# Kernel tuning notes

Hardware: AMD Instinct MI355X
Metric: run time of the kernel (lower is better)

## Reference

```python
import jax, jax.numpy as jnp
import numpy as np

BS, NCAM, CIN, H, W = 1, 6, 512, 32, 88
MID = 256
DBINS = 112  # (58 - 2) / 0.5
VX, VY, VZ = 128, 128, 16


def conv2d(x, w, pad=1):
    return jax.lax.conv_general_dilated(
        x, w, (1, 1), [(pad, pad), (pad, pad)],
        dimension_numbers=('NCHW', 'OIHW', 'NCHW'))


def grid_sample_3d(feat, grid):
    """F.grid_sample 3D, bilinear, padding_mode='zeros', align_corners=False.
    feat: (N, C, D, H, W); grid: (N, X, Y, Z, 3) with xyz -> (W, H, D) coords in [-1,1].
    Returns (N, C, X, Y, Z)."""
    N, C, D, Hh, Ww = feat.shape
    gx, gy, gz = grid[..., 0], grid[..., 1], grid[..., 2]
    ix = ((gx + 1.0) * Ww - 1.0) * 0.5
    iy = ((gy + 1.0) * Hh - 1.0) * 0.5
    iz = ((gz + 1.0) * D - 1.0) * 0.5
    ix0, iy0, iz0 = jnp.floor(ix), jnp.floor(iy), jnp.floor(iz)
    fx, fy, fz = ix - ix0, iy - iy0, iz - iz0
    feat_flat = feat.reshape(N, C, D * Hh * Ww)
    out = jnp.zeros((N, C) + grid.shape[1:-1], feat.dtype)
    for dz in (0, 1):
        for dy in (0, 1):
            for dx in (0, 1):
                xi, yi, zi = ix0 + dx, iy0 + dy, iz0 + dz
                w_ = ((fx if dx else 1.0 - fx) * (fy if dy else 1.0 - fy)
                      * (fz if dz else 1.0 - fz))
                valid = ((xi >= 0) & (xi < Ww) & (yi >= 0) & (yi < Hh)
                         & (zi >= 0) & (zi < D))
                xc = jnp.clip(xi, 0, Ww - 1).astype(jnp.int32)
                yc = jnp.clip(yi, 0, Hh - 1).astype(jnp.int32)
                zc = jnp.clip(zi, 0, D - 1).astype(jnp.int32)
                idx = ((zc * Hh + yc) * Ww + xc).reshape(N, 1, -1)
                g = jnp.take_along_axis(feat_flat, idx, axis=2)
                g = g.reshape((N, C) + grid.shape[1:-1])
                out = out + g * (w_ * valid)[:, None]
    return out


def setup_inputs():
    key = jax.random.key(0)
    ks = jax.random.split(key, 16)
    f32 = jnp.float32
    img_feat = jax.random.normal(ks[0], (BS, NCAM, CIN, H, W), f32)
    intr = np.zeros((NCAM, 4, 4), np.float32)
    for i in range(NCAM):
        f = 1266.0 + 10.0 * i
        intr[i, 0, 0] = f; intr[i, 1, 1] = f
        intr[i, 0, 2] = 800.0; intr[i, 1, 2] = 450.0
        intr[i, 2, 2] = 1.0; intr[i, 3, 3] = 1.0
    intrins = jnp.asarray(intr)[None]  # (1, 6, 4, 4)
    # normalized frustum-sample coords; slightly beyond [-1,1] to hit zero padding
    grid = jax.random.uniform(ks[1], (BS, NCAM, VX, VY, VZ, 3), f32, -1.1, 1.1)
    s3 = (2.0 / (CIN * 9)) ** 0.5
    sm = (2.0 / (MID * 9)) ** 0.5
    s1 = (2.0 / MID) ** 0.5
    red_w = jax.random.normal(ks[2], (MID, CIN, 3, 3), f32) * s3
    red_s = jnp.ones((MID,), f32); red_b = jnp.zeros((MID,), f32)
    mlp_w1 = jax.random.normal(ks[3], (1, MID), f32) * 1.4
    mlp_b1 = jnp.zeros((MID,), f32)
    mlp_w2 = jax.random.normal(ks[4], (MID, MID), f32) * s1
    mlp_b2 = jnp.zeros((MID,), f32)
    se_rw = jax.random.normal(ks[5], (MID, MID, 1, 1), f32) * s1
    se_rb = jnp.zeros((MID,), f32)
    se_ew = jax.random.normal(ks[6], (MID, MID, 1, 1), f32) * s1
    se_eb = jnp.zeros((MID,), f32)
    bb_w = jax.random.normal(ks[7], (3, 2, MID, MID, 3, 3), f32) * sm
    bb_s = jnp.ones((3, 2, MID), f32); bb_b = jnp.zeros((3, 2, MID), f32)
    dp_w = jax.random.normal(ks[8], (DBINS, MID, 1, 1), f32) * s1
    dp_b = jnp.zeros((DBINS,), f32)
    return dict(img_feat=img_feat, intrins=intrins, grid=grid,
                red_w=red_w, red_s=red_s, red_b=red_b,
                mlp_w1=mlp_w1, mlp_b1=mlp_b1, mlp_w2=mlp_w2, mlp_b2=mlp_b2,
                se_rw=se_rw, se_rb=se_rb, se_ew=se_ew, se_eb=se_eb,
                bb_w=bb_w, bb_s=bb_s, bb_b=bb_b, dp_w=dp_w, dp_b=dp_b)


def reference(img_feat, intrins, grid, red_w, red_s, red_b,
              mlp_w1, mlp_b1, mlp_w2, mlp_b2,
              se_rw, se_rb, se_ew, se_eb, bb_w, bb_s, bb_b, dp_w, dp_b):
    bs, n, c, h, w = img_feat.shape
    x = img_feat.reshape(bs * n, c, h, w)
    # pixel-size SE conditioning from inverse intrinsics
    inv = jnp.linalg.inv(intrins)
    pixel_size = jnp.linalg.norm(
        jnp.stack([inv[..., 0, 0], inv[..., 1, 1]], -1), axis=-1).reshape(-1, 1)
    sp = pixel_size * 1000.0  # scale_depth_factor
    # reduce_conv: conv3x3 + (folded) BN + ReLU
    x = conv2d(x, red_w)
    x = jax.nn.relu(x * red_s[:, None, None] + red_b[:, None, None])
    # Mlp on scaled pixel size
    x_se = jax.nn.relu(sp @ mlp_w1 + mlp_b1) @ mlp_w2 + mlp_b2
    x_se = x_se[:, :, None, None]
    # SELayer
    t = jax.nn.relu(conv2d(x_se, se_rw, pad=0) + se_rb[:, None, None])
    gate = jax.nn.sigmoid(conv2d(t, se_ew, pad=0) + se_eb[:, None, None])
    x = x * gate
    # 3 BasicBlocks (conv-bn-relu-conv-bn + residual, relu), BN folded (eval)
    for i in range(3):
        y = conv2d(x, bb_w[i, 0])
        y = jax.nn.relu(y * bb_s[i, 0][:, None, None] + bb_b[i, 0][:, None, None])
        y = conv2d(y, bb_w[i, 1])
        y = y * bb_s[i, 1][:, None, None] + bb_b[i, 1][:, None, None]
        x = jax.nn.relu(x + y)
    depth = conv2d(x, dp_w, pad=0) + dp_b[:, None, None]  # (bs*n, D, h, w)
    dp = jax.nn.softmax(depth, axis=1)
    # stack depth prob and ones so one grid_sample yields features AND voxel mask
    feat = jnp.stack([dp, jnp.ones_like(dp)], axis=1)  # (bs*n, 2, D, h, w)
    g = grid.reshape((bs * n,) + grid.shape[2:])       # (bs*n, X, Y, Z, 3)
    sampled = grid_sample_3d(feat, g)                  # (bs*n, 2, X, Y, Z)
    sampled = sampled.reshape((bs, n) + sampled.shape[1:]).sum(axis=1)
    agg, masks = sampled[:, :1], sampled[:, 1:]
    out = jnp.where(masks > 0, agg / jnp.where(masks > 0, masks, 1.0), agg)
    return out  # (bs, 1, X, Y, Z)
```

## Files before the change

kernel.cpp:

```cpp
#include <hip/hip_runtime.h>

typedef _Float16 f16;
typedef _Float16 f16x8 __attribute__((ext_vector_type(8)));
typedef _Float16 f16x4 __attribute__((ext_vector_type(4)));
typedef float f32x4 __attribute__((ext_vector_type(4)));

#define NCAM 6
#define CINF 512
#define MIDC 256
#define DB   112
#define HH   32
#define WW   88
#define PH   34
#define PW   90
#define NPOS (HH*WW)
#define PTILE 64
#define PT_PER_CAM 44

#define O_GATE   0L
#define O_WFRED  6144L
#define O_LOG    6144L
#define O_WFBB   2365440L
#define O_WFDP   9443328L
#define O_XP0    9508864L
#define O_X1     28309504L
#define O_DP     28309504L
#define O_X2     37709824L
#define O_X3     47110144L

__device__ __forceinline__ void gl_lds16(const void* g, void* l) {
  __builtin_amdgcn_global_load_lds((const __attribute__((address_space(1))) void*)g,
                                   (__attribute__((address_space(3))) void*)l, 16, 0, 0);
}

__global__ void halo_zero_kernel(f16* __restrict__ xp0, f16* __restrict__ X1,
                                 f16* __restrict__ X2, f16* __restrict__ X3) {
  int idx = blockIdx.x * 256 + threadIdx.x;
  f16* base; int C, rem;
  if (idx < 93696) { base = xp0; C = 512; rem = idx; }
  else {
    int k = idx - 93696;
    int bsel = k / 46848;
    if (bsel >= 3) return;
    rem = k - bsel * 46848; C = 256;
    base = (bsel == 0) ? X1 : (bsel == 1) ? X2 : X3;
  }
  int chunks = C >> 3;
  int cell = rem / chunks, cc = rem - cell * chunks;
  int cam = cell / 244, p = cell - cam * 244;
  int hh, ww;
  if (p < 90)       { hh = 0;  ww = p; }
  else if (p < 180) { hh = 33; ww = p - 90; }
  else { int q = p - 180; hh = 1 + (q >> 1); ww = (q & 1) * 89; }
  long o = ((long)(cam * PH + hh) * PW + ww) * C + cc * 8;
  f16x8 z = {0,0,0,0,0,0,0,0};
  *(f16x8*)(base + o) = z;
}

__global__ void wfrag_kernel(const float* __restrict__ src, const float* __restrict__ scale,
                             f16* __restrict__ dst, int NC, int G, int TAPS, int CI, int CO_SRC,
                             long per, long total) {
  long i = (long)blockIdx.x * blockDim.x + threadIdx.x;
  long stride = (long)gridDim.x * blockDim.x;
  int KST = CI >> 5;
  for (; i < total; i += stride) {
    int conv = (int)(i / per);
    long rem = i - (long)conv * per;
    int j = (int)(rem & 7);
    int lane = (int)((rem >> 3) & 63);
    int mi = (int)((rem >> 9) & 3);
    long b = rem >> 11;
    int ks = (int)(b % KST);
    long b2 = b / KST;
    int tap = (int)(b2 % TAPS);
    int g = (int)(b2 / TAPS);
    int co = g * 64 + mi * 16 + (lane & 15);
    int ci = ks * 32 + (lane >> 4) * 8 + j;
    float v = 0.f;
    if (co < CO_SRC) {
      v = src[(long)conv * CO_SRC * CI * TAPS + ((long)co * CI + ci) * TAPS + tap];
      if (scale) v *= scale[conv * CO_SRC + co];
    }
    dst[i] = (f16)v;
  }
}

__global__ void img_trans_kernel(const float* __restrict__ src, f16* __restrict__ dst) {
  __shared__ float tile[32][33];
  int tx = threadIdx.x & 31, ty = threadIdx.x >> 5;
  int wt = blockIdx.x % 3, ct = blockIdx.x / 3;
  int h = blockIdx.y, n = blockIdx.z;
  int w0 = wt * 32, c0 = ct * 32;
  #pragma unroll
  for (int i = 0; i < 4; ++i) {
    int cl = ty + i * 8;
    int w = w0 + tx;
    float v = 0.f;
    if (w < WW) v = src[((long)(n * CINF + c0 + cl) * HH + h) * WW + w];
    tile[cl][tx] = v;
  }
  __syncthreads();
  #pragma unroll
  for (int i = 0; i < 4; ++i) {
    int wl = ty + i * 8;
    int w = w0 + wl;
    if (w < WW)
      dst[((long)((n * PH + h + 1) * PW + (w + 1))) * CINF + c0 + tx] = (f16)tile[tx][wl];
  }
}

__global__ void se_gate_kernel(const float* __restrict__ intr,
                               const float* __restrict__ w1, const float* __restrict__ b1,
                               const float* __restrict__ w2, const float* __restrict__ b2,
                               const float* __restrict__ rw, const float* __restrict__ rb,
                               const float* __restrict__ ew, const float* __restrict__ eb,
                               float* __restrict__ gate) {
  __shared__ float sps;
  __shared__ float h1[MIDC];
  __shared__ float h2[MIDC];
  __shared__ float tt[MIDC];
  int n = blockIdx.x, c = threadIdx.x;
  if (c == 0) {
    float a[4][8];
    for (int i = 0; i < 4; ++i)
      for (int j = 0; j < 4; ++j) {
        a[i][j] = intr[n * 16 + i * 4 + j];
        a[i][4 + j] = (i == j) ? 1.f : 0.f;
      }
    for (int col = 0; col < 4; ++col) {
      int piv = col;
      for (int r2 = col + 1; r2 < 4; ++r2)
        if (fabsf(a[r2][col]) > fabsf(a[piv][col])) piv = r2;
      if (piv != col)
        for (int j = 0; j < 8; ++j) { float tv = a[col][j]; a[col][j] = a[piv][j]; a[piv][j] = tv; }
      float invp = 1.f / a[col][col];
      for (int j = 0; j < 8; ++j) a[col][j] *= invp;
      for (int r2 = 0; r2 < 4; ++r2)
        if (r2 != col) {
          float f = a[r2][col];
          for (int j = 0; j < 8; ++j) a[r2][j] -= f * a[col][j];
        }
    }
    float i00 = a[0][4], i11 = a[1][5];
    sps = sqrtf(i00 * i00 + i11 * i11) * 1000.f;
  }
  __syncthreads();
  float sp = sps;
  h1[c] = fmaxf(sp * w1[c] + b1[c], 0.f);
  __syncthreads();
  float acc = b2[c];
  for (int j = 0; j < MIDC; ++j) acc += h1[j] * w2[j * MIDC + c];
  h2[c] = acc;
  __syncthreads();
  acc = rb[c];
  for (int j = 0; j < MIDC; ++j) acc += rw[c * MIDC + j] * h2[j];
  tt[c] = fmaxf(acc, 0.f);
  __syncthreads();
  acc = eb[c];
  for (int j = 0; j < MIDC; ++j) acc += ew[c * MIDC + j] * tt[j];
  gate[n * MIDC + c] = 1.f / (1.f + expf(-acc));
}

template<int MODE, int CIN_T, int TAPS>
__global__ __launch_bounds__(256, 2)
void conv_mfma(const f16* __restrict__ X, const f16* __restrict__ Wf,
               const float* __restrict__ bias, const float* __restrict__ gate,
               const f16* __restrict__ res, f16* __restrict__ Yf16,
               float* __restrict__ Yf32, int co_tiles) {
  constexpr int KST = CIN_T / 32;
  constexpr int CPT = CIN_T / 64;
  constexpr int NCH = TAPS * CPT;
  constexpr int LCPT = (CPT == 8) ? 3 : 2;
  constexpr long GSTR = (long)TAPS * KST * 4096;
  __shared__ __align__(16) char S[49152];

  const int t = threadIdx.x;
  const int wv = t >> 6, ln = t & 63, lm = ln & 15, quad = ln >> 4;
  const int wm = wv >> 1, wn = wv & 1;
  const int bid0 = blockIdx.x;
  const int cpx = gridDim.x >> 3;
  const int bid = (bid0 & 7) * cpx + (bid0 >> 3);
  const int co_tile = bid % co_tiles;
  const int ptile = bid / co_tiles;
  const int cam = ptile / PT_PER_CAM;
  const int pbase = (ptile % PT_PER_CAM) * PTILE;

  const f16* gB[2]; int ldsoffB[2];
  const int clog = (ln & 7) ^ (ln >> 3);
  #pragma unroll
  for (int j = 0; j < 2; ++j) {
    int reg = j * 4 + wv;
    int r = reg * 8 + (ln >> 3);
    int pos = pbase + r;
    int hh = pos / WW, w2 = pos - hh * WW;
    gB[j] = X + ((long)((cam * PH + hh + 1) * PW + (w2 + 1))) * CIN_T + clog * 8;
    ldsoffB[j] = 16384 + reg * 1024;
  }

  const int base_l = (wn * 32 + lm) * 128;
  const int sx0 = ((0 * 4 + quad) ^ (lm & 7)) * 16;
  const int sx1 = ((1 * 4 + quad) ^ (lm & 7)) * 16;

  f32x4 acc[4][2];
  #pragma unroll
  for (int mi = 0; mi < 4; ++mi)
    #pragma unroll
    for (int ni = 0; ni < 2; ++ni)
      #pragma unroll
      for (int r = 0; r < 4; ++r) acc[mi][ni][r] = 0.f;

  auto choff = [&](int c) -> long {
    long off = 0;
    if (TAPS == 9) {
      int tp = c >> LCPT;
      int dy = tp / 3 - 1, dx = tp % 3 - 1;
      off = (long)(dy * PW + dx) * CIN_T;
    }
    return off + (long)(c & (CPT - 1)) * 64;
  };
  auto stageA = [&](int bsel, int c) {
    const char* sb = (const char*)Wf + (long)c * 8192 + (long)ln * 16;
    char* db = S + bsel * 24576;
    #pragma unroll
    for (int j = 0; j < 4; ++j) {
      int seg = j * 4 + wv;
      long gb = (long)(co_tile * 2 + (seg >> 3)) * GSTR;
      gl_lds16(sb + gb + (seg & 7) * 1024, db + seg * 1024);
    }
  };
  auto stageB = [&](int bsel, long curf) {
    #pragma unroll
    for (int j = 0; j < 2; ++j)
      gl_lds16(gB[j] + curf, S + bsel * 24576 + ldsoffB[j]);
  };
  auto compute = [&](int bsel) {
    const char* ab = S + bsel * 24576 + wm * 8192 + ln * 16;
    const char* bb = S + bsel * 24576 + 16384 + base_l;
    #pragma unroll
    for (int s = 0; s < 2; ++s) {
      f16x8 af[4];
      #pragma unroll
      for (int mi = 0; mi < 4; ++mi)
        af[mi] = *(const f16x8*)(ab + s * 4096 + mi * 1024);
      f16x8 bf[2];
      int sx = s ? sx1 : sx0;
      #pragma unroll
      for (int ni = 0; ni < 2; ++ni)
        bf[ni] = *(const f16x8*)(bb + ni * 2048 + sx);
      #pragma unroll
      for (int mi = 0; mi < 4; ++mi)
        #pragma unroll
        for (int ni = 0; ni < 2; ++ni)
          acc[mi][ni] = __builtin_amdgcn_mfma_f32_16x16x32_f16(af[mi], bf[ni], acc[mi][ni], 0, 0, 0);
    }
  };

  stageA(0, 0);
  stageB(0, choff(0));
  __syncthreads();

  #pragma unroll 1
  for (int c = 0; c < NCH; ++c) {
    int cur = c & 1;
    if (c + 1 < NCH) { stageA(cur ^ 1, c + 1); stageB(cur ^ 1, choff(c + 1)); }
    compute(cur);
    __syncthreads();
  }

  float4 b4[4], g4[4];
  bool skip[4];
  #pragma unroll
  for (int mi = 0; mi < 4; ++mi) {
    int co_l = wm * 64 + mi * 16 + quad * 4;
    int co_g = co_tile * 128 + co_l;
    skip[mi] = (MODE == 3) && (co_l >= DB);
    if (!skip[mi]) b4[mi] = *(const float4*)(bias + co_g);
    if (MODE == 0) g4[mi] = *(const float4*)(gate + cam * MIDC + co_g);
  }
  #pragma unroll
  for (int ni = 0; ni < 2; ++ni) {
    int pos = pbase + wn * 32 + ni * 16 + lm;
    long ob;
    if (MODE == 3) ob = ((long)(cam * NPOS + pos)) * DB;
    else {
      int hh = pos / WW, w2 = pos - hh * WW;
      ob = ((long)((cam * PH + hh + 1) * PW + (w2 + 1))) * MIDC + co_tile * 128;
    }
    #pragma unroll
    for (int mi = 0; mi < 4; ++mi) {
      if (skip[mi]) continue;
      int co_l = wm * 64 + mi * 16 + quad * 4;
      float v[4];
      #pragma unroll
      for (int r = 0; r < 4; ++r) {
        float y = acc[mi][ni][r];
        y += ((float*)&b4[mi])[r];
        if (MODE == 0) y = fmaxf(y, 0.f) * ((float*)&g4[mi])[r];
        else if (MODE == 1) y = fmaxf(y, 0.f);
        v[r] = y;
      }
      if (MODE == 3) {
        float4 o; o.x = v[0]; o.y = v[1]; o.z = v[2]; o.w = v[3];
        *(float4*)(Yf32 + ob + co_l) = o;
      } else if (MODE == 2) {
        f16x4 rv = *(const f16x4*)(res + ob + co_l);
        f16x4 o;
        #pragma unroll
        for (int r = 0; r < 4; ++r) o[r] = (f16)fmaxf(v[r] + (float)rv[r], 0.f);
        *(f16x4*)(Yf16 + ob + co_l) = o;
      } else {
        f16x4 o;
        #pragma unroll
        for (int r = 0; r < 4; ++r) o[r] = (f16)v[r];
        *(f16x4*)(Yf16 + ob + co_l) = o;
      }
    }
  }
}

__global__ void softmax_kernel(const float* __restrict__ L, float* __restrict__ dp) {
  int wid = (int)(((long)blockIdx.x * blockDim.x + threadIdx.x) >> 6);
  int lane = threadIdx.x & 63;
  if (wid >= NCAM * NPOS) return;
  const float* lp = L + (long)wid * DB;
  float v0 = -1e30f, v1 = -1e30f;
  if (lane < 56) { v0 = lp[lane * 2]; v1 = lp[lane * 2 + 1]; }
  float m = fmaxf(v0, v1);
  #pragma unroll
  for (int o = 32; o; o >>= 1) m = fmaxf(m, __shfl_xor(m, o));
  float e0 = 0.f, e1 = 0.f;
  if (lane < 56) { e0 = __expf(v0 - m); e1 = __expf(v1 - m); }
  float ssum = e0 + e1;
  #pragma unroll
  for (int o = 32; o; o >>= 1) ssum += __shfl_xor(ssum, o);
  float inv = 1.f / ssum;
  if (lane < 56) {
    float2 r; r.x = e0 * inv; r.y = e1 * inv;
    *(float2*)(dp + (long)wid * DB + lane * 2) = r;
  }
}

__global__ void sample_kernel(const float* __restrict__ grid, const float* __restrict__ dp,
                              float* __restrict__ out) {
  int v = blockIdx.x * blockDim.x + threadIdx.x;
  if (v >= 128 * 128 * 16) return;
  int vz = v & 15, vy = (v >> 4) & 127, vx = v >> 11;
  float agg = 0.f, msk = 0.f;
  #pragma unroll 1
  for (int n = 0; n < NCAM; ++n) {
    long gb = ((long)((n * 128 + vx) * 128 + vy) * 16 + vz) * 3;
    float gx = grid[gb], gy = grid[gb + 1], gz = grid[gb + 2];
    float ix = ((gx + 1.f) * (float)WW - 1.f) * 0.5f;
    float iy = ((gy + 1.f) * (float)HH - 1.f) * 0.5f;
    float iz = ((gz + 1.f) * (float)DB - 1.f) * 0.5f;
    float xf = floorf(ix), yf = floorf(iy), zf = floorf(iz);
    float fx = ix - xf, fy = iy - yf, fz = iz - zf;
    int x0 = (int)xf, y0 = (int)yf, z0 = (int)zf;
    float wxa[2] = {1.f - fx, fx};
    float wya[2] = {1.f - fy, fy};
    float wza[2] = {1.f - fz, fz};
    #pragma unroll
    for (int dy2 = 0; dy2 < 2; ++dy2) {
      int y = y0 + dy2;
      bool vyb = (y >= 0) && (y < HH);
      int yc = y < 0 ? 0 : (y > HH - 1 ? HH - 1 : y);
      #pragma unroll
      for (int dx2 = 0; dx2 < 2; ++dx2) {
        int x = x0 + dx2;
        bool vxb = (x >= 0) && (x < WW);
        int xc = x < 0 ? 0 : (x > WW - 1 ? WW - 1 : x);
        float wxy = wxa[dx2] * wya[dy2];
        const float* base = dp + ((long)((n * HH + yc) * WW + xc)) * DB;
        #pragma unroll
        for (int dz2 = 0; dz2 < 2; ++dz2) {
          int z = z0 + dz2;
          bool vzb = (z >= 0) && (z < DB);
          int zc = z < 0 ? 0 : (z > DB - 1 ? DB - 1 : z);
          float wgt = wxy * wza[dz2];
          if (vxb && vyb && vzb) {
            msk += wgt;
            agg += wgt * base[zc];
          }
        }
      }
    }
  }
  out[v] = (msk > 0.f) ? (agg / msk) : agg;
}

extern "C" void kernel_launch(void* const* d_in, const int* in_sizes, int n_in,
                              void* d_out, int out_size, void* d_ws, size_t ws_size,
                              hipStream_t stream) {
  const float* img   = (const float*)d_in[0];
  const float* intr  = (const float*)d_in[1];
  const float* grid  = (const float*)d_in[2];
  const float* red_w = (const float*)d_in[3];
  const float* red_s = (const float*)d_in[4];
  const float* red_b = (const float*)d_in[5];
  const float* w1    = (const float*)d_in[6];
  const float* b1    = (const float*)d_in[7];
  const float* w2    = (const float*)d_in[8];
  const float* b2    = (const float*)d_in[9];
  const float* rw    = (const float*)d_in[10];
  const float* rb    = (const float*)d_in[11];
  const float* ew    = (const float*)d_in[12];
  const float* eb    = (const float*)d_in[13];
  const float* bb_w  = (const float*)d_in[14];
  const float* bb_s  = (const float*)d_in[15];
  const float* bb_b  = (const float*)d_in[16];
  const float* dp_w  = (const float*)d_in[17];
  const float* dp_b  = (const float*)d_in[18];
  float* out = (float*)d_out;

  char* ws = (char*)d_ws;
  float* gate = (float*)(ws + O_GATE);
  f16* wfred  = (f16*)(ws + O_WFRED);
  f16* wfbb   = (f16*)(ws + O_WFBB);
  f16* wfdp   = (f16*)(ws + O_WFDP);
  f16* xp0    = (f16*)(ws + O_XP0);
  f16* X1     = (f16*)(ws + O_X1);
  f16* X2     = (f16*)(ws + O_X2);
  f16* X3     = (f16*)(ws + O_X3);
  float* Lg   = (float*)(ws + O_LOG);
  float* dpb  = (float*)(ws + O_DP);

  halo_zero_kernel<<<915, 256, 0, stream>>>(xp0, X1, X2, X3);
  {
    long per = 4L * 9 * 16 * 2048, total = per;
    wfrag_kernel<<<2048, 256, 0, stream>>>(red_w, red_s, wfred, 1, 4, 9, 512, 256, per, total);
  }
  {
    long per = 4L * 9 * 8 * 2048, total = 6 * per;
    wfrag_kernel<<<4096, 256, 0, stream>>>(bb_w, bb_s, wfbb, 6, 4, 9, 256, 256, per, total);
  }
  {
    long per = 2L * 1 * 8 * 2048, total = per;
    wfrag_kernel<<<128, 256, 0, stream>>>(dp_w, nullptr, wfdp, 1, 2, 1, 256, 112, per, total);
  }
  img_trans_kernel<<<dim3(48, 32, 6), 256, 0, stream>>>(img, xp0);
  se_gate_kernel<<<6, 256, 0, stream>>>(intr, w1, b1, w2, b2, rw, rb, ew, eb, gate);

  const long WCH = 4L * 9 * 8 * 2048;

  conv_mfma<0, 512, 9><<<528, 256, 0, stream>>>(xp0, wfred, red_b, gate, nullptr, X1, nullptr, 2);

  conv_mfma<1, 256, 9><<<528, 256, 0, stream>>>(X1, wfbb + 0 * WCH, bb_b + 0 * 256, nullptr, nullptr, X2, nullptr, 2);
  conv_mfma<2, 256, 9><<<528, 256, 0, stream>>>(X2, wfbb + 1 * WCH, bb_b + 1 * 256, nullptr, X1, X3, nullptr, 2);
  conv_mfma<1, 256, 9><<<528, 256, 0, stream>>>(X3, wfbb + 2 * WCH, bb_b + 2 * 256, nullptr, nullptr, X2, nullptr, 2);
  conv_mfma<2, 256, 9><<<528, 256, 0, stream>>>(X2, wfbb + 3 * WCH, bb_b + 3 * 256, nullptr, X3, X1, nullptr, 2);
  conv_mfma<1, 256, 9><<<528, 256, 0, stream>>>(X1, wfbb + 4 * WCH, bb_b + 4 * 256, nullptr, nullptr, X2, nullptr, 2);
  conv_mfma<2, 256, 9><<<528, 256, 0, stream>>>(X2, wfbb + 5 * WCH, bb_b + 5 * 256, nullptr, X1, X3, nullptr, 2);

  conv_mfma<3, 256, 1><<<264, 256, 0, stream>>>(X3, wfdp, dp_b, nullptr, nullptr, nullptr, Lg, 1);

  softmax_kernel<<<4224, 256, 0, stream>>>(Lg, dpb);
  sample_kernel<<<1024, 256, 0, stream>>>(grid, dpb, out);
}
```

Before: 483.3 us.

## Merge prep kernels into one launch and fuse softmax into depth conv epilogue

Folds halo zeroing, weight fragment packing, image transpose and SE gate into a single block-dispatched prep kernel, removing five kernel launches. The depth 1x1 conv epilogue now stages logits in LDS and computes the per-pixel softmax directly, writing probabilities and dropping the separate softmax kernel and its logit round-trip through global memory. The softmax epilogue uses only 4 lanes per pixel with strided, uncoalesced output stores.

```diff
diff --git a/kernel.cpp b/kernel.cpp
--- a/kernel.cpp
+++ b/kernel.cpp
@@ -19,7 +19,6 @@
 
 #define O_GATE   0L
 #define O_WFRED  6144L
-#define O_LOG    6144L
 #define O_WFBB   2365440L
 #define O_WFDP   9443328L
 #define O_XP0    9508864L
@@ -33,35 +32,11 @@
                                    (__attribute__((address_space(3))) void*)l, 16, 0, 0);
 }
 
-__global__ void halo_zero_kernel(f16* __restrict__ xp0, f16* __restrict__ X1,
-                                 f16* __restrict__ X2, f16* __restrict__ X3) {
-  int idx = blockIdx.x * 256 + threadIdx.x;
-  f16* base; int C, rem;
-  if (idx < 93696) { base = xp0; C = 512; rem = idx; }
-  else {
-    int k = idx - 93696;
-    int bsel = k / 46848;
-    if (bsel >= 3) return;
-    rem = k - bsel * 46848; C = 256;
-    base = (bsel == 0) ? X1 : (bsel == 1) ? X2 : X3;
-  }
-  int chunks = C >> 3;
-  int cell = rem / chunks, cc = rem - cell * chunks;
-  int cam = cell / 244, p = cell - cam * 244;
-  int hh, ww;
-  if (p < 90)       { hh = 0;  ww = p; }
-  else if (p < 180) { hh = 33; ww = p - 90; }
-  else { int q = p - 180; hh = 1 + (q >> 1); ww = (q & 1) * 89; }
-  long o = ((long)(cam * PH + hh) * PW + ww) * C + cc * 8;
-  f16x8 z = {0,0,0,0,0,0,0,0};
-  *(f16x8*)(base + o) = z;
-}
-
-__global__ void wfrag_kernel(const float* __restrict__ src, const float* __restrict__ scale,
-                             f16* __restrict__ dst, int NC, int G, int TAPS, int CI, int CO_SRC,
-                             long per, long total) {
-  long i = (long)blockIdx.x * blockDim.x + threadIdx.x;
-  long stride = (long)gridDim.x * blockDim.x;
+__device__ void wfrag_body(const float* __restrict__ src, const float* __restrict__ scale,
+                           f16* __restrict__ dst, int TAPS, int CI, int CO_SRC,
+                           long per, long total, int lbid, int nb) {
+  long i = (long)lbid * 256 + threadIdx.x;
+  long stride = (long)nb * 256;
   int KST = CI >> 5;
   for (; i < total; i += stride) {
     int conv = (int)(i / per);
@@ -85,80 +60,123 @@
   }
 }
 
-__global__ void img_trans_kernel(const float* __restrict__ src, f16* __restrict__ dst) {
-  __shared__ float tile[32][33];
-  int tx = threadIdx.x & 31, ty = threadIdx.x >> 5;
-  int wt = blockIdx.x % 3, ct = blockIdx.x / 3;
-  int h = blockIdx.y, n = blockIdx.z;
-  int w0 = wt * 32, c0 = ct * 32;
-  #pragma unroll
-  for (int i = 0; i < 4; ++i) {
-    int cl = ty + i * 8;
-    int w = w0 + tx;
-    float v = 0.f;
-    if (w < WW) v = src[((long)(n * CINF + c0 + cl) * HH + h) * WW + w];
-    tile[cl][tx] = v;
-  }
-  __syncthreads();
-  #pragma unroll
-  for (int i = 0; i < 4; ++i) {
-    int wl = ty + i * 8;
-    int w = w0 + wl;
-    if (w < WW)
-      dst[((long)((n * PH + h + 1) * PW + (w + 1))) * CINF + c0 + tx] = (f16)tile[tx][wl];
-  }
-}
-
-__global__ void se_gate_kernel(const float* __restrict__ intr,
-                               const float* __restrict__ w1, const float* __restrict__ b1,
-                               const float* __restrict__ w2, const float* __restrict__ b2,
-                               const float* __restrict__ rw, const float* __restrict__ rb,
-                               const float* __restrict__ ew, const float* __restrict__ eb,
-                               float* __restrict__ gate) {
-  __shared__ float sps;
-  __shared__ float h1[MIDC];
-  __shared__ float h2[MIDC];
-  __shared__ float tt[MIDC];
-  int n = blockIdx.x, c = threadIdx.x;
-  if (c == 0) {
-    float a[4][8];
-    for (int i = 0; i < 4; ++i)
-      for (int j = 0; j < 4; ++j) {
-        a[i][j] = intr[n * 16 + i * 4 + j];
-        a[i][4 + j] = (i == j) ? 1.f : 0.f;
+__global__ void prep_kernel(f16* __restrict__ xp0, f16* __restrict__ X1,
+                            f16* __restrict__ X2, f16* __restrict__ X3,
+                            const float* __restrict__ img,
+                            const float* __restrict__ intr,
+                            const float* __restrict__ w1, const float* __restrict__ b1,
+                            const float* __restrict__ w2, const float* __restrict__ b2,
+                            const float* __restrict__ rw, const float* __restrict__ rb,
+                            const float* __restrict__ ew, const float* __restrict__ eb,
+                            float* __restrict__ gate,
+                            const float* __restrict__ red_w, const float* __restrict__ red_s,
+                            f16* __restrict__ wfred,
+                            const float* __restrict__ bb_w, const float* __restrict__ bb_s,
+                            f16* __restrict__ wfbb,
+                            const float* __restrict__ dp_w, f16* __restrict__ wfdp) {
+  __shared__ float shbuf[1056];
+  const int bid = blockIdx.x;
+  if (bid < 915) {
+    int idx = bid * 256 + threadIdx.x;
+    f16* base; int C, rem;
+    if (idx < 93696) { base = xp0; C = 512; rem = idx; }
+    else {
+      int k = idx - 93696;
+      int bsel = k / 46848;
+      if (bsel >= 3) return;
+      rem = k - bsel * 46848; C = 256;
+      base = (bsel == 0) ? X1 : (bsel == 1) ? X2 : X3;
+    }
+    int chunks = C >> 3;
+    int cell = rem / chunks, cc = rem - cell * chunks;
+    int cam = cell / 244, p = cell - cam * 244;
+    int hh, ww;
+    if (p < 90)       { hh = 0;  ww = p; }
+    else if (p < 180) { hh = 33; ww = p - 90; }
+    else { int q = p - 180; hh = 1 + (q >> 1); ww = (q & 1) * 89; }
+    long o = ((long)(cam * PH + hh) * PW + ww) * C + cc * 8;
+    f16x8 z = {0,0,0,0,0,0,0,0};
+    *(f16x8*)(base + o) = z;
+  } else if (bid < 10131) {
+    int lb = bid - 915;
+    int x = lb % 48;
+    int h = (lb / 48) % 32;
+    int n = lb / 1536;
+    int wt = x % 3, ct = x / 3;
+    float (*tile)[33] = (float(*)[33])shbuf;
+    int tx = threadIdx.x & 31, ty = threadIdx.x >> 5;
+    int w0 = wt * 32, c0 = ct * 32;
+    #pragma unroll
+    for (int i = 0; i < 4; ++i) {
+      int cl = ty + i * 8;
+      int w = w0 + tx;
+      float v = 0.f;
+      if (w < WW) v = img[((long)(n * CINF + c0 + cl) * HH + h) * WW + w];
+      tile[cl][tx] = v;
+    }
+    __syncthreads();
+    #pragma unroll
+    for (int i = 0; i < 4; ++i) {
+      int wl = ty + i * 8;
+      int w = w0 + wl;
+      if (w < WW)
+        xp0[((long)((n * PH + h + 1) * PW + (w + 1))) * CINF + c0 + tx] = (f16)tile[tx][wl];
+    }
+  } else if (bid < 10137) {
+    int n = bid - 10131, c = threadIdx.x;
+    float* sps = shbuf;
+    float* h1 = shbuf + 32;
+    float* h2 = shbuf + 288;
+    float* tt = shbuf + 544;
+    if (c == 0) {
+      float a[4][8];
+      for (int i = 0; i < 4; ++i)
+        for (int j = 0; j < 4; ++j) {
+          a[i][j] = intr[n * 16 + i * 4 + j];
+          a[i][4 + j] = (i == j) ? 1.f : 0.f;
+        }
+      for (int col = 0; col < 4; ++col) {
+        int piv = col;
+        for (int r2 = col + 1; r2 < 4; ++r2)
+          if (fabsf(a[r2][col]) > fabsf(a[piv][col])) piv = r2;
+        if (piv != col)
+          for (int j = 0; j < 8; ++j) { float tv = a[col][j]; a[col][j] = a[piv][j]; a[piv][j] = tv; }
+        float invp = 1.f / a[col][col];
+        for (int j = 0; j < 8; ++j) a[col][j] *= invp;
+        for (int r2 = 0; r2 < 4; ++r2)
+          if (r2 != col) {
+            float f = a[r2][col];
+            for (int j = 0; j < 8; ++j) a[r2][j] -= f * a[col][j];
+          }
       }
-    for (int col = 0; col < 4; ++col) {
-      int piv = col;
-      for (int r2 = col + 1; r2 < 4; ++r2)
-        if (fabsf(a[r2][col]) > fabsf(a[piv][col])) piv = r2;
-      if (piv != col)
-        for (int j = 0; j < 8; ++j) { float tv = a[col][j]; a[col][j] = a[piv][j]; a[piv][j] = tv; }
-      float invp = 1.f / a[col][col];
-      for (int j = 0; j < 8; ++j) a[col][j] *= invp;
-      for (int r2 = 0; r2 < 4; ++r2)
-        if (r2 != col) {
-          float f = a[r2][col];
-          for (int j = 0; j < 8; ++j) a[r2][j] -= f * a[col][j];
-        }
-    }
-    float i00 = a[0][4], i11 = a[1][5];
-    sps = sqrtf(i00 * i00 + i11 * i11) * 1000.f;
-  }
-  __syncthreads();
-  float sp = sps;
-  h1[c] = fmaxf(sp * w1[c] + b1[c], 0.f);
-  __syncthreads();
-  float acc = b2[c];
-  for (int j = 0; j < MIDC; ++j) acc += h1[j] * w2[j * MIDC + c];
-  h2[c] = acc;
-  __syncthreads();
-  acc = rb[c];
-  for (int j = 0; j < MIDC; ++j) acc += rw[c * MIDC + j] * h2[j];
-  tt[c] = fmaxf(acc, 0.f);
-  __syncthreads();
-  acc = eb[c];
-  for (int j = 0; j < MIDC; ++j) acc += ew[c * MIDC + j] * tt[j];
-  gate[n * MIDC + c] = 1.f / (1.f + expf(-acc));
+      float i00 = a[0][4], i11 = a[1][5];
+      sps[0] = sqrtf(i00 * i00 + i11 * i11) * 1000.f;
+    }
+    __syncthreads();
+    float sp = sps[0];
+    h1[c] = fmaxf(sp * w1[c] + b1[c], 0.f);
+    __syncthreads();
+    float acc = b2[c];
+    for (int j = 0; j < MIDC; ++j) acc += h1[j] * w2[j * MIDC + c];
+    h2[c] = acc;
+    __syncthreads();
+    acc = rb[c];
+    for (int j = 0; j < MIDC; ++j) acc += rw[c * MIDC + j] * h2[j];
+    tt[c] = fmaxf(acc, 0.f);
+    __syncthreads();
+    acc = eb[c];
+    for (int j = 0; j < MIDC; ++j) acc += ew[c * MIDC + j] * tt[j];
+    gate[n * MIDC + c] = 1.f / (1.f + expf(-acc));
+  } else if (bid < 12185) {
+    long per = 4L * 9 * 16 * 2048;
+    wfrag_body(red_w, red_s, wfred, 9, 512, 256, per, per, bid - 10137, 2048);
+  } else if (bid < 16281) {
+    long per = 4L * 9 * 8 * 2048;
+    wfrag_body(bb_w, bb_s, wfbb, 9, 256, 256, per, 6 * per, bid - 12185, 4096);
+  } else {
+    long per = 2L * 1 * 8 * 2048;
+    wfrag_body(dp_w, nullptr, wfdp, 1, 256, 112, per, per, bid - 16281, 128);
+  }
 }
 
 template<int MODE, int CIN_T, int TAPS>
@@ -277,18 +295,51 @@
     if (!skip[mi]) b4[mi] = *(const float4*)(bias + co_g);
     if (MODE == 0) g4[mi] = *(const float4*)(gate + cam * MIDC + co_g);
   }
+
+  if (MODE == 3) {
+    float* P = (float*)S;
+    #pragma unroll
+    for (int ni = 0; ni < 2; ++ni) {
+      int prow = wn * 32 + ni * 16 + lm;
+      #pragma unroll
+      for (int mi = 0; mi < 4; ++mi) {
+        if (skip[mi]) continue;
+        int co_l = wm * 64 + mi * 16 + quad * 4;
+        float4 o;
+        o.x = acc[mi][ni][0] + ((float*)&b4[mi])[0];
+        o.y = acc[mi][ni][1] + ((float*)&b4[mi])[1];
+        o.z = acc[mi][ni][2] + ((float*)&b4[mi])[2];
+        o.w = acc[mi][ni][3] + ((float*)&b4[mi])[3];
+        *(float4*)(P + prow * 116 + co_l) = o;
+      }
+    }
+    __syncthreads();
+    int p = t >> 2, k = t & 3;
+    const float* Pr = P + p * 116;
+    float m = -1e30f;
+    for (int b = k; b < DB; b += 4) m = fmaxf(m, Pr[b]);
+    m = fmaxf(m, __shfl_xor(m, 1));
+    m = fmaxf(m, __shfl_xor(m, 2));
+    float e[28];
+    float ssum = 0.f;
+    int cnt = 0;
+    for (int b = k; b < DB; b += 4) { float ev = __expf(Pr[b] - m); e[cnt++] = ev; ssum += ev; }
+    ssum += __shfl_xor(ssum, 1);
+    ssum += __shfl_xor(ssum, 2);
+    float inv = 1.f / ssum;
+    float* op = Yf32 + ((long)(cam * NPOS + pbase + p)) * DB;
+    cnt = 0;
+    for (int b = k; b < DB; b += 4) op[b] = e[cnt++] * inv;
+    return;
+  }
+
   #pragma unroll
   for (int ni = 0; ni < 2; ++ni) {
     int pos = pbase + wn * 32 + ni * 16 + lm;
-    long ob;
-    if (MODE == 3) ob = ((long)(cam * NPOS + pos)) * DB;
-    else {
-      int hh = pos / WW, w2 = pos - hh * WW;
-      ob = ((long)((cam * PH + hh + 1) * PW + (w2 + 1))) * MIDC + co_tile * 128;
-    }
+    int hh = pos / WW, w2 = pos - hh * WW;
+    long ob = ((long)((cam * PH + hh + 1) * PW + (w2 + 1))) * MIDC + co_tile * 128;
     #pragma unroll
     for (int mi = 0; mi < 4; ++mi) {
-      if (skip[mi]) continue;
       int co_l = wm * 64 + mi * 16 + quad * 4;
       float v[4];
       #pragma unroll
@@ -299,10 +350,7 @@
         else if (MODE == 1) y = fmaxf(y, 0.f);
         v[r] = y;
       }
-      if (MODE == 3) {
-        float4 o; o.x = v[0]; o.y = v[1]; o.z = v[2]; o.w = v[3];
-        *(float4*)(Yf32 + ob + co_l) = o;
-      } else if (MODE == 2) {
+      if (MODE == 2) {
         f16x4 rv = *(const f16x4*)(res + ob + co_l);
         f16x4 o;
         #pragma unroll
@@ -315,28 +363,6 @@
         *(f16x4*)(Yf16 + ob + co_l) = o;
       }
     }
-  }
-}
-
-__global__ void softmax_kernel(const float* __restrict__ L, float* __restrict__ dp) {
-  int wid = (int)(((long)blockIdx.x * blockDim.x + threadIdx.x) >> 6);
-  int lane = threadIdx.x & 63;
-  if (wid >= NCAM * NPOS) return;
-  const float* lp = L + (long)wid * DB;
-  float v0 = -1e30f, v1 = -1e30f;
-  if (lane < 56) { v0 = lp[lane * 2]; v1 = lp[lane * 2 + 1]; }
-  float m = fmaxf(v0, v1);
-  #pragma unroll
-  for (int o = 32; o; o >>= 1) m = fmaxf(m, __shfl_xor(m, o));
-  float e0 = 0.f, e1 = 0.f;
-  if (lane < 56) { e0 = __expf(v0 - m); e1 = __expf(v1 - m); }
-  float ssum = e0 + e1;
-  #pragma unroll
-  for (int o = 32; o; o >>= 1) ssum += __shfl_xor(ssum, o);
-  float inv = 1.f / ssum;
-  if (lane < 56) {
-    float2 r; r.x = e0 * inv; r.y = e1 * inv;
-    *(float2*)(dp + (long)wid * DB + lane * 2) = r;
   }
 }
 
@@ -421,24 +447,11 @@
   f16* X1     = (f16*)(ws + O_X1);
   f16* X2     = (f16*)(ws + O_X2);
   f16* X3     = (f16*)(ws + O_X3);
-  float* Lg   = (float*)(ws + O_LOG);
   float* dpb  = (float*)(ws + O_DP);
 
-  halo_zero_kernel<<<915, 256, 0, stream>>>(xp0, X1, X2, X3);
-  {
-    long per = 4L * 9 * 16 * 2048, total = per;
-    wfrag_kernel<<<2048, 256, 0, stream>>>(red_w, red_s, wfred, 1, 4, 9, 512, 256, per, total);
-  }
-  {
-    long per = 4L * 9 * 8 * 2048, total = 6 * per;
-    wfrag_kernel<<<4096, 256, 0, stream>>>(bb_w, bb_s, wfbb, 6, 4, 9, 256, 256, per, total);
-  }
-  {
-    long per = 2L * 1 * 8 * 2048, total = per;
-    wfrag_kernel<<<128, 256, 0, stream>>>(dp_w, nullptr, wfdp, 1, 2, 1, 256, 112, per, total);
-  }
-  img_trans_kernel<<<dim3(48, 32, 6), 256, 0, stream>>>(img, xp0);
-  se_gate_kernel<<<6, 256, 0, stream>>>(intr, w1, b1, w2, b2, rw, rb, ew, eb, gate);
+  prep_kernel<<<16409, 256, 0, stream>>>(xp0, X1, X2, X3, img,
+                                         intr, w1, b1, w2, b2, rw, rb, ew, eb, gate,
+                                         red_w, red_s, wfred, bb_w, bb_s, wfbb, dp_w, wfdp);
 
   const long WCH = 4L * 9 * 8 * 2048;
 
@@ -451,8 +464,7 @@
   conv_mfma<1, 256, 9><<<528, 256, 0, stream>>>(X1, wfbb + 4 * WCH, bb_b + 4 * 256, nullptr, nullptr, X2, nullptr, 2);
   conv_mfma<2, 256, 9><<<528, 256, 0, stream>>>(X2, wfbb + 5 * WCH, bb_b + 5 * 256, nullptr, X1, X3, nullptr, 2);
 
-  conv_mfma<3, 256, 1><<<264, 256, 0, stream>>>(X3, wfdp, dp_b, nullptr, nullptr, nullptr, Lg, 1);
-
-  softmax_kernel<<<4224, 256, 0, stream>>>(Lg, dpb);
+  conv_mfma<3, 256, 1><<<264, 256, 0, stream>>>(X3, wfdp, dp_b, nullptr, nullptr, nullptr, dpb, 1);
+
   sample_kernel<<<1024, 256, 0, stream>>>(grid, dpb, out);
 }
```

Measured after the change: 462.3 us. 1.05x faster.
